# Kernel tuning notes

Measured on AMD Instinct MI355X. Metric: run time of the kernel, lower is better.

The kernel has to match this reference:

```python
import jax, jax.numpy as jnp
import numpy as np

B, S, H, N, D = 2, 2048, 1024, 16, 64  # batch, seq, hidden, heads, head_size
PAD = -30000.0


def setup_inputs() -> dict:
    key = jax.random.key(0)
    kx, kqkv, kout, krpe = jax.random.split(key, 4)
    x = jax.random.normal(kx, (B, S, H), jnp.float32)
    qkv = jax.random.normal(kqkv, (H, 3, N, D), jnp.float32) * H ** (-0.5)
    out_w = jax.random.normal(kout, (N, D, H), jnp.float32) * (N * D) ** (-0.5)
    # rpe_bias is zero-init in torch; use small randn so the bias path is exercised
    rpe_bias = jax.random.normal(krpe, (N, S), jnp.float32) * 0.02
    return {"x": x, "qkv": qkv, "out_w": out_w, "rpe_bias": rpe_bias}


def reference(x, qkv, out_w, rpe_bias):
    # q, k, v: [B, N, S, D]
    q, k, v = jnp.einsum('bsx,xMnd->Mbnsd', x, qkv)
    s = x.shape[1]
    a = jnp.einsum('bnsd,bntd->bnst', q, k) * q.shape[-1] ** (-0.5)
    # cumulative relative-position bias: bias[n, i, j] = cumsum(rpe)[n, i-j] for i>=j,
    # PAD otherwise (exactly what to_tril produces on the row-broadcast cumsum).
    cum = jnp.cumsum(rpe_bias[:, :s], axis=-1)            # [N, S]
    rel = jnp.arange(s)[:, None] - jnp.arange(s)[None, :]  # [S, S], i - j
    bias = jnp.where(rel >= 0, cum[:, jnp.clip(rel, 0)], PAD)  # [N, S, S]
    a = jax.nn.softmax(a + bias, axis=-1)
    mix = jnp.einsum('bnst,bntd->bnsd', a, v)
    return jnp.einsum('bnsd,ndx->bsx', mix, out_w)
```

## Files before the change

### kernel.cpp

```cpp
#include <hip/hip_runtime.h>
#include <hip/hip_bf16.h>
#include <cstdint>
#include <cstddef>

#define B_   2
#define S_   2048
#define H_   1024
#define NH   16
#define DH   64
#define LOG2E 1.4426950408889634f
#define SCALE2 (0.125f * LOG2E)

typedef __hip_bfloat16 bf16;
typedef short bf16x8 __attribute__((ext_vector_type(8)));
typedef float f32x4 __attribute__((ext_vector_type(4)));

#define MFMA16(a, b, c) __builtin_amdgcn_mfma_f32_16x16x32_bf16((a), (b), (c), 0, 0, 0)

__device__ __forceinline__ void async16(const void* g, void* l) {
  __builtin_amdgcn_global_load_lds(
      (const __attribute__((address_space(1))) void*)g,
      (__attribute__((address_space(3))) void*)l,
      16, 0, 0);
}
__device__ __forceinline__ void async4(const void* g, void* l) {
  __builtin_amdgcn_global_load_lds(
      (const __attribute__((address_space(1))) void*)g,
      (__attribute__((address_space(3))) void*)l,
      4, 0, 0);
}

__device__ __forceinline__ short bf16bits(float v) {
  bf16 t = __float2bfloat16(v);
  return *reinterpret_cast<short*>(&t);
}

__device__ __forceinline__ void tr_body(const float* __restrict__ src,
                                        bf16* __restrict__ dst, int R, int C,
                                        int c0, int r0, bf16 (*tile)[33], int tid) {
  int tx = tid & 31, ty = tid >> 5;
  for (int i = 0; i < 32; i += 8)
    tile[ty + i][tx] = __float2bfloat16(src[(size_t)(r0 + ty + i) * C + c0 + tx]);
  __syncthreads();
  for (int i = 0; i < 32; i += 8)
    dst[(size_t)(c0 + ty + i) * R + r0 + tx] = tile[tx][ty + i];
}

__global__ __launch_bounds__(256)
void prep(const float* __restrict__ x, bf16* __restrict__ xb,
          const float* __restrict__ qkv, bf16* __restrict__ qkvT,
          const float* __restrict__ outw, bf16* __restrict__ outwT,
          const float* __restrict__ rpe, float* __restrict__ cum) {
  __shared__ char pm[2176] __attribute__((aligned(16)));
  const int L = blockIdx.x, tid = threadIdx.x;
  if (L < 4096) {
    int i = (L * 256 + tid) * 4;
    float4 v = *(const float4*)(x + i);
    bf16 o[4] = {__float2bfloat16(v.x), __float2bfloat16(v.y),
                 __float2bfloat16(v.z), __float2bfloat16(v.w)};
    *(uint64_t*)(xb + i) = *(const uint64_t*)o;
  } else if (L < 7168) {
    int t = L - 4096;
    int cx = t % 96, ry = t / 96;
    tr_body(qkv, qkvT, 1024, 3072, cx * 32, ry * 32, (bf16(*)[33])pm, tid);
  } else if (L < 8192) {
    int t = L - 7168;
    int cx = t & 31, ry = t >> 5;
    tr_body(outw, outwT, 1024, 1024, cx * 32, ry * 32, (bf16(*)[33])pm, tid);
  } else {
    float* ssum = (float*)pm;
    int n = L - 8192;
    float loc[8];
    float s = 0.f;
    int base = tid * 8;
#pragma unroll
    for (int u = 0; u < 8; ++u) {
      loc[u] = rpe[n * S_ + base + u];
      s += loc[u];
    }
    ssum[tid] = s;
    __syncthreads();
    float own = s;
    for (int off = 1; off < 256; off <<= 1) {
      float v = (tid >= off) ? ssum[tid - off] : 0.f;
      __syncthreads();
      ssum[tid] += v;
      __syncthreads();
    }
    float run = ssum[tid] - own;
#pragma unroll
    for (int u = 0; u < 8; ++u) {
      run += loc[u];
      cum[n * S_ + base + u] = run * LOG2E;
    }
  }
}

template <int MODE>
__global__ __launch_bounds__(256, MODE == 0 ? 3 : 2)
void gemm_bt(const bf16* __restrict__ A, const bf16* __restrict__ Bt,
             bf16* __restrict__ C0, bf16* __restrict__ C1, bf16* __restrict__ C2,
             float* __restrict__ F0) {
  constexpr int NT = (MODE == 0) ? 4 : 2;
  constexpr int NB = NT * 32;
  __shared__ char smem[MODE == 0 ? 36864 : 24576] __attribute__((aligned(16)));
  bf16* As = (bf16*)smem;
  bf16* Bs = (bf16*)(smem + 16384);
  const int tid = threadIdx.x, lane = tid & 63, w = tid >> 6;
  const int lr = lane & 15, lq = lane >> 4;
  const int m0 = blockIdx.y * 128, n0 = blockIdx.x * NB;
  const int wm = (w & 1) * 64, wn = (w >> 1) * (NT * 16);

  f32x4 acc[4][NT] = {};

  for (int k0 = 0; k0 < 1024; k0 += 64) {
    __syncthreads();
#pragma unroll
    for (int t = 0; t < 4; ++t) {
      int c = t * 256 + tid;
      int row = c >> 3, ch = c & 7;
      int cs = ch ^ (row & 7);
      async16(A + (size_t)(m0 + row) * 1024 + k0 + cs * 8,
              (char*)As + c * 16);
    }
#pragma unroll
    for (int t = 0; t < NB / 32; ++t) {
      int c = t * 256 + tid;
      int row = c >> 3, ch = c & 7;
      int cs = ch ^ (row & 7);
      async16(Bt + (size_t)(n0 + row) * 1024 + k0 + cs * 8,
              (char*)Bs + c * 16);
    }
    __syncthreads();
    bf16x8 af[4][2], bfr[NT][2];
#pragma unroll
    for (int mt = 0; mt < 4; ++mt) {
      int row = wm + mt * 16 + lr;
#pragma unroll
      for (int kt = 0; kt < 2; ++kt)
        af[mt][kt] = *(const bf16x8*)(As + row * 64 +
                         (((kt * 4 + lq) ^ (row & 7)) << 3));
    }
#pragma unroll
    for (int nt = 0; nt < NT; ++nt) {
      int row = wn + nt * 16 + lr;
#pragma unroll
      for (int kt = 0; kt < 2; ++kt)
        bfr[nt][kt] = *(const bf16x8*)(Bs + row * 64 +
                          (((kt * 4 + lq) ^ (row & 7)) << 3));
    }
#pragma unroll
    for (int mt = 0; mt < 4; ++mt)
#pragma unroll
      for (int nt = 0; nt < NT; ++nt)
#pragma unroll
        for (int kt = 0; kt < 2; ++kt)
          acc[mt][nt] = MFMA16(af[mt][kt], bfr[nt][kt], acc[mt][nt]);
  }

  if (MODE == 0) {
    __syncthreads();
    bf16* E = (bf16*)smem + w * (64 * 72);
    const int cbase = n0 + wn;
    const int mm = cbase >> 10, nn = (cbase >> 6) & 15;
    const int bb = (m0 + wm) >> 11;
    const int sbase = (m0 + wm) & 2047;
    if (mm < 2) {
#pragma unroll
      for (int mt = 0; mt < 4; ++mt)
#pragma unroll
        for (int nt = 0; nt < 4; ++nt)
#pragma unroll
          for (int r = 0; r < 4; ++r)
            E[(mt * 16 + lq * 4 + r) * 72 + nt * 16 + lr] =
                __float2bfloat16(acc[mt][nt][r]);
      bf16* dst = (mm == 0 ? C0 : C1) +
                  ((size_t)(bb * NH + nn) * S_ + sbase) * DH;
#pragma unroll
      for (int it = 0; it < 8; ++it) {
        int c = it * 64 + lane;
        int rw = c >> 3, c8 = c & 7;
        *(uint4*)(dst + (size_t)rw * DH + c8 * 8) =
            *(const uint4*)(E + rw * 72 + c8 * 8);
      }
    } else {
#pragma unroll
      for (int mt = 0; mt < 4; ++mt)
#pragma unroll
        for (int nt = 0; nt < 4; ++nt)
#pragma unroll
          for (int r = 0; r < 4; ++r)
            E[(nt * 16 + lr) * 72 + mt * 16 + lq * 4 + r] =
                __float2bfloat16(acc[mt][nt][r]);
      bf16* dst = C2 + (size_t)(bb * NH + nn) * DH * S_;
#pragma unroll
      for (int it = 0; it < 8; ++it) {
        int c = it * 64 + lane;
        int dr = c >> 3, c8 = c & 7;
        *(uint4*)(dst + (size_t)dr * S_ + sbase + c8 * 8) =
            *(const uint4*)(E + dr * 72 + c8 * 8);
      }
    }
  } else {
#pragma unroll
    for (int mt = 0; mt < 4; ++mt)
#pragma unroll
      for (int nt = 0; nt < NT; ++nt)
#pragma unroll
        for (int r = 0; r < 4; ++r) {
          int rM = m0 + wm + mt * 16 + lq * 4 + r;
          int cN = n0 + wn + nt * 16 + lr;
          F0[(size_t)rM * 1024 + cN] = acc[mt][nt][r];
        }
  }
}

__device__ __forceinline__ void fa_stage(const bf16* __restrict__ k,
                                         const bf16* __restrict__ vt,
                                         const float* __restrict__ cumn,
                                         char* smem, int bn, int i0, int jb,
                                         int buf, int tid) {
  char* dst = smem + buf * 32768;
  const char* ksrc = (const char*)(k + ((size_t)bn * S_ + jb) * DH);
#pragma unroll
  for (int t = 0; t < 4; ++t) {
    int c = t * 256 + tid;
    int row = c >> 3, ch = c & 7;
    int cs = ch ^ ((row & 3) | ((row >> 1) & 4));
    async16(ksrc + row * 128 + cs * 16, dst + c * 16);
  }
  const char* vsrc = (const char*)(vt + (size_t)bn * DH * S_);
#pragma unroll
  for (int t = 0; t < 4; ++t) {
    int c = t * 256 + tid;
    int row = c >> 4, ch = c & 15;
    int cs = ch ^ (row & 15);
    async16(vsrc + (size_t)row * (S_ * 2) + jb * 2 + cs * 16,
            dst + 16384 + c * 16);
  }
  if (tid < 194) {
    float* cdst = (float*)(smem + 65536) + buf * 800;
    int base = i0 - jb - 127 + tid;
#pragma unroll
    for (int p = 0; p < 4; ++p) {
      int src = base + p;
      src = src < 0 ? 0 : (src > S_ - 1 ? S_ - 1 : src);
      async4(cumn + src, cdst + p * 200 + tid);
    }
  }
}

__global__ __launch_bounds__(256, 2)
void fa_kernel(const bf16* __restrict__ q, const bf16* __restrict__ k,
               const bf16* __restrict__ vt, const float* __restrict__ cum,
               bf16* __restrict__ mix) {
  __shared__ char smem[72192] __attribute__((aligned(16)));
  float* combL = (float*)(smem + 71936);

  const int tid = threadIdx.x, lane = tid & 63, w = tid >> 6;
  const int lr = lane & 15, lq = lane >> 4;
  const int rg = w & 1, jh = w >> 1;

  const int L = blockIdx.x;
  const int xcd = L & 7, slot = L >> 3;
  const int bn = xcd + 8 * (slot & 3);
  const int pp = slot >> 2;
  const int n = bn & (NH - 1);
  const int b = bn >> 4;
  const float* cumn = cum + n * S_;

  const int T0 = 31 - pp;
  const int T1 = pp;
  const int nu0 = (T0 + 2) >> 1;

  bf16x8 ones;
#pragma unroll
  for (int u = 0; u < 8; ++u) ones[u] = (short)0x3F80;
  const f32x4 fz = {0.f, 0.f, 0.f, 0.f};

  const int kkey = (lr & 3) | (((lr >> 2) & 1) << 2);

  bf16x8 qf[2][2];
  f32x4 oacc[2][4];
  f32x4 lacc[2];

  fa_stage(k, vt, cumn, smem, bn, T0 * 64, 0, 0, tid);

  int ti = T0, jt = 0, i0 = T0 * 64, nu = nu0;

  for (int g = 0; g < 17; ++g) {
    const int bsel = g & 1;
    const char* kb = smem + bsel * 32768;
    const char* vb = kb + 16384;
    const float* cumB = (const float*)(smem + 65536) + bsel * 800;
    const int jb = jt * 128;
    const bool diag = (jt == nu - 1);

    __syncthreads();

    if (g + 1 < 17) {
      int gn = g + 1, tin, jtn;
      if (gn < nu0) { tin = T0; jtn = gn; }
      else          { tin = T1; jtn = gn - nu0; }
      fa_stage(k, vt, cumn, smem, bn, tin * 64, jtn * 128, bsel ^ 1, tid);
    }

    if (jt == 0) {
      const bf16* qbase = q + ((size_t)bn * S_ + i0 + rg * 32) * DH;
#pragma unroll
      for (int is = 0; is < 2; ++is) {
#pragma unroll
        for (int kd = 0; kd < 2; ++kd)
          qf[is][kd] = *(const bf16x8*)(qbase + (is * 16 + lr) * DH + kd * 32 + lq * 8);
        lacc[is] = fz;
#pragma unroll
        for (int dt = 0; dt < 4; ++dt) oacc[is][dt] = fz;
      }
    }

    f32x4 sa[2][4] = {};
#pragma unroll
    for (int kd = 0; kd < 2; ++kd)
#pragma unroll
      for (int mm = 0; mm < 4; ++mm) {
        int kt = mm >> 1, nt2 = mm & 1;
        int krow = jh * 64 + kt * 32 + ((lr >> 2) << 3) + nt2 * 4 + (lr & 3);
        bf16x8 kf = *(const bf16x8*)(kb + krow * 128 +
                        (((kd * 4 + lq) ^ kkey) << 4));
        sa[0][mm] = MFMA16(kf, qf[0][kd], sa[0][mm]);
        sa[1][mm] = MFMA16(kf, qf[1][kd], sa[1][mm]);
      }

    const int doff = i0 - jb;
    bf16x8 pf[2][2];
#pragma unroll
    for (int is = 0; is < 2; ++is) {
      const int ilocI = rg * 32 + is * 16 + lr;
#pragma unroll
      for (int mm = 0; mm < 4; ++mm) {
        int kt = mm >> 1, nt2 = mm & 1;
        int jl = jh * 64 + kt * 32 + lq * 8 + nt2 * 4;
        int Xm3 = 124 + ilocI - jl;
        int ph = Xm3 & 3, b0 = Xm3 & ~3;
        f32x4 cv = *(const f32x4*)(cumB + ph * 200 + b0);
        if (!diag) {
#pragma unroll
          for (int r = 0; r < 4; ++r)
            pf[is][kt][nt2 * 4 + r] =
                bf16bits(exp2f(sa[is][mm][r] * SCALE2 + cv[3 - r]));
        } else {
#pragma unroll
          for (int r = 0; r < 4; ++r) {
            float pv = (doff + ilocI - jl - r >= 0)
                           ? exp2f(sa[is][mm][r] * SCALE2 + cv[3 - r])
                           : 0.f;
            pf[is][kt][nt2 * 4 + r] = bf16bits(pv);
          }
        }
      }
    }

#pragma unroll
    for (int kt = 0; kt < 2; ++kt) {
      lacc[0] = MFMA16(pf[0][kt], ones, lacc[0]);
      lacc[1] = MFMA16(pf[1][kt], ones, lacc[1]);
#pragma unroll
      for (int dt = 0; dt < 4; ++dt) {
        int vrow = dt * 16 + lr;
        bf16x8 vf = *(const bf16x8*)(vb + vrow * 256 +
                        (((jh * 8 + kt * 4 + lq) ^ (vrow & 15)) << 4));
        oacc[0][dt] = MFMA16(pf[0][kt], vf, oacc[0][dt]);
        oacc[1][dt] = MFMA16(pf[1][kt], vf, oacc[1][dt]);
      }
    }

    if (diag) {
      __syncthreads();
      float* scr = (float*)(smem + bsel * 32768) + rg * 2048;
      if (jh == 1) {
#pragma unroll
        for (int is = 0; is < 2; ++is) {
#pragma unroll
          for (int dt = 0; dt < 4; ++dt)
#pragma unroll
            for (int r = 0; r < 4; ++r) {
              int row = is * 16 + lq * 4 + r;
              int col = ((dt ^ lq) << 4) + lr;
              scr[row * 64 + col] = oacc[is][dt][r];
            }
          if (lr == 0)
#pragma unroll
            for (int r = 0; r < 4; ++r)
              combL[rg * 32 + is * 16 + lq * 4 + r] = lacc[is][r];
        }
      }
      __syncthreads();
      if (jh == 0) {
#pragma unroll
        for (int is = 0; is < 2; ++is) {
#pragma unroll
          for (int r = 0; r < 4; ++r)
            lacc[is][r] += combL[rg * 32 + is * 16 + lq * 4 + r];
#pragma unroll
          for (int dt = 0; dt < 4; ++dt)
#pragma unroll
            for (int r = 0; r < 4; ++r) {
              int row = is * 16 + lq * 4 + r;
              int col = ((dt ^ lq) << 4) + lr;
              oacc[is][dt][r] += scr[row * 64 + col];
            }
        }
#pragma unroll
        for (int is = 0; is < 2; ++is)
#pragma unroll
          for (int dt = 0; dt < 4; ++dt)
#pragma unroll
            for (int r = 0; r < 4; ++r) {
              int i = i0 + rg * 32 + is * 16 + lq * 4 + r;
              int d = dt * 16 + lr;
              mix[((size_t)(b * S_ + i) * NH + n) * DH + d] =
                  __float2bfloat16(oacc[is][dt][r] / lacc[is][r]);
            }
      }
      ti = T1; jt = 0; i0 = T1 * 64; nu = (T1 + 2) >> 1;
    } else {
      ++jt;
    }
  }
}

extern "C" void kernel_launch(void* const* d_in, const int* in_sizes, int n_in,
                              void* d_out, int out_size, void* d_ws, size_t ws_size,
                              hipStream_t stream) {
  const float* x     = (const float*)d_in[0];
  const float* qkv   = (const float*)d_in[1];
  const float* out_w = (const float*)d_in[2];
  const float* rpe   = (const float*)d_in[3];
  float* out = (float*)d_out;

  char* ws = (char*)d_ws;
  bf16* qkvT  = (bf16*)(ws + 0);
  bf16* outwT = (bf16*)(ws + 6291456);
  bf16* xb    = (bf16*)(ws + 8388608);
  bf16* qb    = (bf16*)(ws + 16777216);
  bf16* kb    = (bf16*)(ws + 25165824);
  bf16* vtb   = (bf16*)(ws + 33554432);
  bf16* mixb  = (bf16*)(ws + 41943040);
  float* cum  = (float*)(ws + 50331648);

  prep<<<8208, 256, 0, stream>>>(x, xb, qkv, qkvT, out_w, outwT, rpe, cum);
  gemm_bt<0><<<dim3(3072 / 128, 4096 / 128), 256, 0, stream>>>(xb, qkvT, qb, kb, vtb, nullptr);
  fa_kernel<<<512, 256, 0, stream>>>(qb, kb, vtb, cum, mixb);
  gemm_bt<1><<<dim3(1024 / 64, 4096 / 128), 256, 0, stream>>>(mixb, outwT, nullptr, nullptr, nullptr, out);
}
```

Before: 178.5 us.

## Double-buffer GEMM LDS tiles with K=32 stages to overlap loads

Restructures the bf16 GEMM main loop into a two-buffer pipeline. The K step drops from 64 to 32 so both buffers fit in the existing shared-memory allocation, and the XOR swizzle is adapted to the narrower rows. The next tile's async global-to-LDS loads are issued before computing on the current tile, so load latency is meant to hide behind the MFMAs. In exchange the loop runs twice as many iterations, each with fewer MFMAs per barrier, and correctness depends on the barrier also waiting for the outstanding async loads.

```diff
diff --git a/kernel.cpp b/kernel.cpp
--- a/kernel.cpp
+++ b/kernel.cpp
@@ -103,9 +103,8 @@
              float* __restrict__ F0) {
   constexpr int NT = (MODE == 0) ? 4 : 2;
   constexpr int NB = NT * 32;
+  constexpr int BUFSZ = 8192 + NB * 64;
   __shared__ char smem[MODE == 0 ? 36864 : 24576] __attribute__((aligned(16)));
-  bf16* As = (bf16*)smem;
-  bf16* Bs = (bf16*)(smem + 16384);
   const int tid = threadIdx.x, lane = tid & 63, w = tid >> 6;
   const int lr = lane & 15, lq = lane >> 4;
   const int m0 = blockIdx.y * 128, n0 = blockIdx.x * NB;
@@ -113,49 +112,50 @@
 
   f32x4 acc[4][NT] = {};
 
-  for (int k0 = 0; k0 < 1024; k0 += 64) {
+  auto stage = [&](int buf, int k0) {
+    char* dst = smem + buf * BUFSZ;
+#pragma unroll
+    for (int t = 0; t < 2; ++t) {
+      int c = t * 256 + tid;
+      int row = c >> 2, ch = c & 3;
+      int k8 = (ch ^ ((row >> 1) & 3)) * 8;
+      async16(A + (size_t)(m0 + row) * 1024 + k0 + k8, dst + c * 16);
+    }
+#pragma unroll
+    for (int t = 0; t < NB / 64; ++t) {
+      int c = t * 256 + tid;
+      int row = c >> 2, ch = c & 3;
+      int k8 = (ch ^ ((row >> 1) & 3)) * 8;
+      async16(Bt + (size_t)(n0 + row) * 1024 + k0 + k8, dst + 8192 + c * 16);
+    }
+  };
+
+  stage(0, 0);
+
+  for (int s = 0; s < 32; ++s) {
+    const int bsel = s & 1;
     __syncthreads();
-#pragma unroll
-    for (int t = 0; t < 4; ++t) {
-      int c = t * 256 + tid;
-      int row = c >> 3, ch = c & 7;
-      int cs = ch ^ (row & 7);
-      async16(A + (size_t)(m0 + row) * 1024 + k0 + cs * 8,
-              (char*)As + c * 16);
-    }
-#pragma unroll
-    for (int t = 0; t < NB / 32; ++t) {
-      int c = t * 256 + tid;
-      int row = c >> 3, ch = c & 7;
-      int cs = ch ^ (row & 7);
-      async16(Bt + (size_t)(n0 + row) * 1024 + k0 + cs * 8,
-              (char*)Bs + c * 16);
-    }
-    __syncthreads();
-    bf16x8 af[4][2], bfr[NT][2];
+
+    if (s + 1 < 32) stage(bsel ^ 1, (s + 1) * 32);
+
+    const bf16* As = (const bf16*)(smem + bsel * BUFSZ);
+    const bf16* Bs = (const bf16*)(smem + bsel * BUFSZ + 8192);
+    bf16x8 af[4], bfr[NT];
 #pragma unroll
     for (int mt = 0; mt < 4; ++mt) {
       int row = wm + mt * 16 + lr;
-#pragma unroll
-      for (int kt = 0; kt < 2; ++kt)
-        af[mt][kt] = *(const bf16x8*)(As + row * 64 +
-                         (((kt * 4 + lq) ^ (row & 7)) << 3));
+      af[mt] = *(const bf16x8*)(As + row * 32 + ((lq ^ ((row >> 1) & 3)) << 3));
     }
 #pragma unroll
     for (int nt = 0; nt < NT; ++nt) {
       int row = wn + nt * 16 + lr;
-#pragma unroll
-      for (int kt = 0; kt < 2; ++kt)
-        bfr[nt][kt] = *(const bf16x8*)(Bs + row * 64 +
-                          (((kt * 4 + lq) ^ (row & 7)) << 3));
+      bfr[nt] = *(const bf16x8*)(Bs + row * 32 + ((lq ^ ((row >> 1) & 3)) << 3));
     }
 #pragma unroll
     for (int mt = 0; mt < 4; ++mt)
 #pragma unroll
       for (int nt = 0; nt < NT; ++nt)
-#pragma unroll
-        for (int kt = 0; kt < 2; ++kt)
-          acc[mt][nt] = MFMA16(af[mt][kt], bfr[nt][kt], acc[mt][nt]);
+        acc[mt][nt] = MFMA16(af[mt], bfr[nt], acc[mt][nt]);
   }
 
   if (MODE == 0) {
```

Result: no change. 178.3 us (-0.2%).
